# Kernel optimization log

Measured on AMD Instinct MI355X. Metric: run time of the kernel, lower is better.

The kernel has to match this reference:

```python
import jax, jax.numpy as jnp
import numpy as np

B, T, H, TYPE = 32, 512, 1024, 32


def setup_inputs() -> dict:
    key = jax.random.key(0)
    ks = jax.random.split(key, 8)
    s = 0.02
    return {
        "event_seqs": jax.random.randint(ks[0], (B, T), 0, TYPE + 1),
        "time_seqs": jax.random.uniform(ks[1], (B, T), jnp.float32),
        "rec_W": jax.random.normal(ks[2], (2 * H, 7 * H), jnp.float32) * s,
        "rec_b": jnp.zeros((7 * H,), jnp.float32),
        "emb": jax.random.normal(ks[3], (TYPE + 1, H), jnp.float32) * s,
        "w1_W": jax.random.normal(ks[4], (H, H), jnp.float32) * s,
        "w1_b": jnp.zeros((H,), jnp.float32),
        "w2_W": jax.random.normal(ks[5], (H, H), jnp.float32) * s,
        "w2_b": jnp.zeros((H,), jnp.float32),
    }


def reference(event_seqs, time_seqs, rec_W, rec_b, emb, w1_W, w1_b, w2_W, w2_b):
    b, t = event_seqs.shape
    h = emb.shape[1]

    def recurrence(feed_emb, h_d, c_tm1, c_bar_tm1):
        # Linear(2H -> 7H) then gate nonlinearities
        g = jnp.concatenate([feed_emb, h_d], axis=1) @ rec_W + rec_b
        gi, gf, gz, go, gib, gfb, gd = jnp.split(g, 7, axis=-1)
        gz = jnp.tanh(gz)
        c_t = jax.nn.sigmoid(gf) * c_tm1 + jax.nn.sigmoid(gi) * gz
        c_bar_t = jax.nn.sigmoid(gfb) * c_bar_tm1 + jax.nn.sigmoid(gib) * gz
        return c_t, c_bar_t, jax.nn.sigmoid(go), jax.nn.softplus(gd)

    zeros = jnp.zeros((b, h), rec_W.dtype)
    emb0 = jnp.broadcast_to(emb[0], (b, h))  # event_embeddings(zeros)
    carry0 = recurrence(emb0, zeros, zeros, zeros)  # (c, c_bar, o, delta)

    emb_seq = emb[event_seqs].swapaxes(0, 1)  # [T, B, H]
    dur_seq = time_seqs.T                      # [T, B]

    def step(carry, xs):
        c, c_bar, o, delta = carry
        e_t, dur_t = xs
        # exponential decay toward c_bar over the elapsed duration
        c_d = c_bar + (c - c_bar) * jnp.exp(-delta * dur_t[:, None])
        h_d = o * jnp.tanh(c_d)
        return recurrence(e_t, h_d, c_d, c_bar), h_d

    _, h_seq = jax.lax.scan(step, carry0, (emb_seq, dur_seq))  # h_seq: [T, B, H]

    h_last = h_seq[-1]  # last timestep hidden (h.transpose(0,1)[:, -1, :])
    hid = jax.nn.relu(h_last @ w1_W + w1_b)  # dropout = identity (eval)
    return hid @ w2_W + w2_b
```

## Files before the change

### kernel.cpp

```cpp
#include <hip/hip_runtime.h>


#define H   1024
#define B   32
#define T   512
#define NG  7
#define C7  7168
#define K2  2048
#define NWG 256

typedef __attribute__((ext_vector_type(4))) float f32x4;

__device__ __attribute__((aligned(16))) float g_Wt[(size_t)C7 * K2];
__device__ __attribute__((aligned(16))) float g_w1t[(size_t)H * H];
__device__ __attribute__((aligned(16))) float g_w2t[(size_t)H * H];
__device__ __attribute__((aligned(16))) float g_embp[(size_t)33 * C7];
__device__ __attribute__((aligned(16))) float g_hbuf[2][B * H];
__device__ __attribute__((aligned(16))) float g_cd[B * H];
__device__ __attribute__((aligned(16))) float g_cb[B * H];

__device__ __forceinline__ float sig_f(float x){
  return __builtin_amdgcn_rcpf(1.f + __builtin_amdgcn_exp2f(-1.44269504089f * x));
}
__device__ __forceinline__ float tanh_f(float x){
  float t = __builtin_amdgcn_exp2f(2.88539008178f * x);
  return 1.f - 2.f * __builtin_amdgcn_rcpf(t + 1.f);
}
__device__ __forceinline__ float softplus_f(float x){
  float p = __builtin_amdgcn_exp2f(-1.44269504089f * fabsf(x));
  return fmaxf(x, 0.f) + 0.69314718056f * __builtin_amdgcn_logf(1.f + p);
}

template<int C>
__device__ __forceinline__ float dppadd(float a){
  int t = __builtin_amdgcn_mov_dpp(__float_as_int(a), C, 0xF, 0xF, true);
  return a + __int_as_float(t);
}
__device__ __forceinline__ float row16_sum(float a){
  a = dppadd<0xB1>(a);
  a = dppadd<0x4E>(a);
  a = dppadd<0x141>(a);
  a = dppadd<0x140>(a);
  return a;
}

__device__ __forceinline__ float d4(f32x4 a, f32x4 b, float s){
  s = __builtin_fmaf(a.x, b.x, s); s = __builtin_fmaf(a.y, b.y, s);
  s = __builtin_fmaf(a.z, b.z, s); s = __builtin_fmaf(a.w, b.w, s);
  return s;
}

__device__ __forceinline__ void loadrow(const float* src, int ln, f32x4 hv[4]){
  const f32x4* p = (const f32x4*)src;
  #pragma unroll
  for (int i = 0; i < 4; ++i) hv[i] = p[i * 64 + ln];
}

__device__ __forceinline__ void load_wslice(const float* Wbase, int colb, int ln,
                                            int kofs, f32x4 w[NG][4]){
  #pragma unroll
  for (int g = 0; g < NG; ++g){
    const float* cp = Wbase + (size_t)(g * H + colb) * K2 + kofs;
    #pragma unroll
    for (int i = 0; i < 4; ++i) w[g][i] = *(const f32x4*)(cp + (i * 64 + ln) * 4);
  }
}

__device__ __forceinline__ void row_partial(const f32x4 hv[4], const f32x4 w[NG][4],
                                            float* gp, int bi, int wv, int ln){
  float a[NG];
  #pragma unroll
  for (int g = 0; g < NG; ++g){
    float s = 0.f;
    #pragma unroll
    for (int i = 0; i < 4; ++i) s = d4(hv[i], w[g][i], s);
    a[g] = row16_sum(s);
  }
  int m = ln & 15;
  float v = a[0];
  v = (m==1)?a[1]:v; v = (m==2)?a[2]:v; v = (m==3)?a[3]:v;
  v = (m==4)?a[4]:v; v = (m==5)?a[5]:v; v = (m==6)?a[6]:v;
  if (m < NG) gp[bi * 112 + wv * 28 + m * 4 + (ln >> 4)] = v;
}

template<int NR>
__device__ __forceinline__ void mm_block(const float* src, const f32x4 w[NG][4],
                                         float* gp, int wv, int ln){
  f32x4 ha[4], hb[4];
  loadrow(src, ln, ha);
  #pragma unroll
  for (int b = 0; b < NR; b += 2){
    if (b + 1 < NR) loadrow(src + (b + 1) * H, ln, hb);
    row_partial(ha, w, gp, b, wv, ln);
    if (b + 2 < NR) loadrow(src + (b + 2) * H, ln, ha);
    if (b + 1 < NR) row_partial(hb, w, gp, b + 1, wv, ln);
  }
}


extern "C" __global__ void __launch_bounds__(256)
transpose_k(const float* __restrict__ in, int which, int R, int C){
  __shared__ float tls[64 * 65];
  float* out = (which == 0) ? g_Wt : (which == 1 ? g_w1t : g_w2t);
  int tx = threadIdx.x & 63, ty = threadIdx.x >> 6;
  size_t c0 = (size_t)blockIdx.x * 64, r0 = (size_t)blockIdx.y * 64;
  #pragma unroll
  for (int i = 0; i < 16; ++i){
    int r = i * 4 + ty;
    tls[r * 65 + tx] = in[(r0 + r) * (size_t)C + c0 + tx];
  }
  __syncthreads();
  #pragma unroll
  for (int i = 0; i < 16; ++i){
    int c = i * 4 + ty;
    out[(c0 + c) * (size_t)R + r0 + tx] = tls[tx * 65 + c];
  }
}

extern "C" __global__ void __launch_bounds__(256, 1)
embproj_k(const float* __restrict__ emb, const float* __restrict__ recb){
  __shared__ float gp[33 * 112];
  int tid = threadIdx.x, wg = blockIdx.x, wv = tid >> 6, ln = tid & 63;
  int colb = wg * 4 + wv;
  f32x4 w[NG][4];
  load_wslice(g_Wt, colb, ln, 0, w);
  mm_block<33>(emb, w, gp, wv, ln);
  __syncthreads();
  for (int idx = tid; idx < 33 * 4; idx += 256){
    int e = idx >> 2, hl = idx & 3, col = wg * 4 + hl;
    #pragma unroll
    for (int g = 0; g < NG; ++g){
      const float* pp = gp + e * 112 + hl * 28 + g * 4;
      g_embp[(size_t)e * C7 + g * H + col] =
          recb[g * H + col] + ((pp[0] + pp[1]) + (pp[2] + pp[3]));
    }
  }
}

extern "C" __global__ void __launch_bounds__(256)
init_k(const float* __restrict__ tm){
  int tid = threadIdx.x, wg = blockIdx.x;
  if (tid < 128){
    int b = tid >> 2, hl = tid & 3, col = wg * 4 + hl, si = b * H + col;
    float G[NG];
    #pragma unroll
    for (int g = 0; g < NG; ++g) G[g] = g_embp[(size_t)g * H + col];
    float gz = tanh_f(G[2]);
    float c  = sig_f(G[0]) * gz;
    float cb = sig_f(G[4]) * gz;
    float dd = softplus_f(G[6]);
    float dur = tm[b * T];
    float cd = cb + (c - cb) * __builtin_amdgcn_exp2f(-1.44269504089f * dd * dur);
    g_cd[si] = cd; g_cb[si] = cb;
    g_hbuf[0][si] = sig_f(G[3]) * tanh_f(cd);
  }
}

extern "C" __global__ void __launch_bounds__(256, 1)
step_k(int t, const int* __restrict__ ev, const float* __restrict__ tm){
  __shared__ float gp[B * 112];
  int tid = threadIdx.x, wg = blockIdx.x, wv = tid >> 6, ln = tid & 63;
  int colb = wg * 4 + wv;
  f32x4 w[NG][4];
  load_wslice(g_Wt, colb, ln, H, w);
  const float* hprev = g_hbuf[(t - 1) & 1];
  mm_block<B>(hprev, w, gp, wv, ln);
  __syncthreads();
  if (tid < 128){
    int b = tid >> 2, hl = tid & 3, col = wg * 4 + hl, si = b * H + col;
    int e = ev[b * T + t - 1];
    const float* ep = g_embp + (size_t)e * C7 + col;
    float G[NG];
    #pragma unroll
    for (int g = 0; g < NG; ++g){
      const float* pp = gp + b * 112 + hl * 28 + g * 4;
      G[g] = ep[(size_t)g * H] + ((pp[0] + pp[1]) + (pp[2] + pp[3]));
    }
    float gz  = tanh_f(G[2]);
    float cdp = g_cd[si], cbp = g_cb[si];
    float c   = sig_f(G[1]) * cdp + sig_f(G[0]) * gz;
    float cb  = sig_f(G[5]) * cbp + sig_f(G[4]) * gz;
    float dd  = softplus_f(G[6]);
    float dur = tm[b * T + t];
    float cd  = cb + (c - cb) * __builtin_amdgcn_exp2f(-1.44269504089f * dd * dur);
    g_cd[si] = cd; g_cb[si] = cb;
    g_hbuf[t & 1][si] = sig_f(G[3]) * tanh_f(cd);
  }
}

extern "C" __global__ void __launch_bounds__(256, 1)
mlp_k(int phase, const float* __restrict__ bias, float* __restrict__ outp){
  __shared__ float gp[B * 16];
  int tid = threadIdx.x, wg = blockIdx.x, wv = tid >> 6, ln = tid & 63;
  int colb = wg * 4 + wv;
  const float* Wt   = phase ? g_w2t : g_w1t;
  const float* hsrc = phase ? g_hbuf[0] : g_hbuf[1];
  f32x4 w[4];
  #pragma unroll
  for (int i = 0; i < 4; ++i)
    w[i] = *(const f32x4*)(Wt + (size_t)colb * H + (i * 64 + ln) * 4);
  #pragma unroll 2
  for (int b = 0; b < B; ++b){
    f32x4 hv[4]; loadrow(hsrc + b * H, ln, hv);
    float s = 0.f;
    #pragma unroll
    for (int i = 0; i < 4; ++i) s = d4(hv[i], w[i], s);
    s = row16_sum(s);
    if ((ln & 15) == 0) gp[b * 16 + wv * 4 + (ln >> 4)] = s;
  }
  __syncthreads();
  if (tid < 128){
    int b = tid >> 2, hl = tid & 3, col = wg * 4 + hl;
    const float* pp = gp + b * 16 + hl * 4;
    float s = ((pp[0] + pp[1]) + (pp[2] + pp[3])) + bias[col];
    if (!phase) g_hbuf[0][b * H + col] = fmaxf(s, 0.f);
    else        outp[b * H + col] = s;
  }
}

extern "C" void kernel_launch(void* const* d_in, const int* in_sizes, int n_in,
                              void* d_out, int out_size, void* d_ws, size_t ws_size,
                              hipStream_t stream)
{
  const int*   ev = (const int*)  d_in[0];
  const float* tm = (const float*)d_in[1];
  const float* rW = (const float*)d_in[2];
  const float* rb = (const float*)d_in[3];
  const float* em = (const float*)d_in[4];
  const float* w1 = (const float*)d_in[5];
  const float* b1 = (const float*)d_in[6];
  const float* w2 = (const float*)d_in[7];
  const float* b2 = (const float*)d_in[8];
  float* outp = (float*)d_out;
  (void)d_ws; (void)ws_size; (void)in_sizes; (void)n_in; (void)out_size;

  dim3 blk(256);
  hipLaunchKernelGGL(transpose_k, dim3(C7 / 64, K2 / 64), blk, 0, stream, rW, 0, K2, C7);
  hipLaunchKernelGGL(transpose_k, dim3(H / 64, H / 64),  blk, 0, stream, w1, 1, H, H);
  hipLaunchKernelGGL(transpose_k, dim3(H / 64, H / 64),  blk, 0, stream, w2, 2, H, H);
  hipLaunchKernelGGL(embproj_k, dim3(NWG), blk, 0, stream, em, rb);
  hipLaunchKernelGGL(init_k,    dim3(NWG), blk, 0, stream, tm);
  for (int t = 1; t < T; ++t)
    hipLaunchKernelGGL(step_k, dim3(NWG), blk, 0, stream, t, ev, tm);
  hipLaunchKernelGGL(mlp_k, dim3(NWG), blk, 0, stream, 0, b1, outp);
  hipLaunchKernelGGL(mlp_k, dim3(NWG), blk, 0, stream, 1, b2, outp);
}
```

Before: 8.040 ms.

## Replace per-timestep launches with a persistent kernel using flag-based grid barriers

Adds a single persistent kernel that runs all timesteps plus the final MLP. Recurrent weights stay in registers and state stays in LDS across steps, with a spin-flag barrier between workgroups in place of 511 separate kernel launches. It reads weights straight from the untransposed inputs with strided loads, which drops the transpose passes. The spin barrier assumes all 256 workgroups are co-resident, and it has a bounded spin count that could silently break correctness if they are not. The old multi-kernel path remains only as a fallback when the launch fails.

```diff
diff --git a/kernel.cpp b/kernel.cpp
--- a/kernel.cpp
+++ b/kernel.cpp
@@ -18,6 +18,7 @@
 __device__ __attribute__((aligned(16))) float g_hbuf[2][B * H];
 __device__ __attribute__((aligned(16))) float g_cd[B * H];
 __device__ __attribute__((aligned(16))) float g_cb[B * H];
+__device__ unsigned g_flags[NWG];
 
 __device__ __forceinline__ float sig_f(float x){
   return __builtin_amdgcn_rcpf(1.f + __builtin_amdgcn_exp2f(-1.44269504089f * x));
@@ -66,6 +67,20 @@
   }
 }
 
+__device__ __forceinline__ void load_w_direct(const float* recW, int colb, int ln,
+                                              int kofs, f32x4 w[NG][4]){
+  #pragma unroll
+  for (int g = 0; g < NG; ++g)
+    #pragma unroll
+    for (int i = 0; i < 4; ++i){
+      const float* base = recW + (size_t)(kofs + i * 256 + ln * 4) * C7 + g * H + colb;
+      w[g][i].x = base[0];
+      w[g][i].y = base[C7];
+      w[g][i].z = base[2 * C7];
+      w[g][i].w = base[3 * C7];
+    }
+}
+
 __device__ __forceinline__ void row_partial(const f32x4 hv[4], const f32x4 w[NG][4],
                                             float* gp, int bi, int wv, int ln){
   float a[NG];
@@ -97,11 +112,180 @@
   }
 }
 
+__device__ __forceinline__ void flag_barrier(unsigned target, int tid, int bid){
+  __syncthreads();
+  if (tid == 0){
+    __threadfence();
+    __hip_atomic_store(&g_flags[bid], target, __ATOMIC_RELAXED,
+                       __HIP_MEMORY_SCOPE_AGENT);
+  }
+  for (int spin = 0; spin < 32768; ++spin){
+    unsigned v = __hip_atomic_load(&g_flags[tid], __ATOMIC_RELAXED,
+                                   __HIP_MEMORY_SCOPE_AGENT);
+    if ((int)(v - target) >= 0) break;
+    __builtin_amdgcn_s_sleep(1);
+  }
+  __threadfence();
+  __syncthreads();
+}
+
+#define P_TM   0
+#define TMS    520
+#define P_EMBP (32*TMS)
+#define P_GP   (P_EMBP + 33*28)
+#define P_CC   (P_GP + 33*112)
+#define P_CB   (P_CC + 128)
+#define P_OO   (P_CB + 128)
+#define P_DD   (P_OO + 128)
+#define P_CDL  (P_DD + 128)
+#define DYN_LDS_BYTES (21904 * 4)
+
+extern "C" __global__ void __launch_bounds__(256, 1)
+ctlstm_persist(const int* __restrict__ ev, const float* __restrict__ tm,
+               const float* __restrict__ recW, const float* __restrict__ recb,
+               const float* __restrict__ emb,  const float* __restrict__ w1W,
+               const float* __restrict__ w1b,  const float* __restrict__ w2W,
+               const float* __restrict__ w2b,  float* __restrict__ out)
+{
+  extern __shared__ float lds[];
+  const int tid = threadIdx.x, wg = blockIdx.x;
+  const int wv = tid >> 6, ln = tid & 63;
+  const int colb = wg * 4 + wv;
+
+  const unsigned base = __hip_atomic_load(&g_flags[tid], __ATOMIC_RELAXED,
+                                          __HIP_MEMORY_SCOPE_AGENT);
+  unsigned bk = 0;
+
+  for (int i = tid; i < B * T; i += 256){
+    int b = i >> 9, t = i & 511;
+    lds[P_TM + b * TMS + t] = tm[i];
+  }
+
+  f32x4 w[NG][4];
+
+  load_w_direct(recW, colb, ln, 0, w);
+  __syncthreads();
+  mm_block<33>(emb, w, lds + P_GP, wv, ln);
+  __syncthreads();
+  for (int idx = tid; idx < 33 * 4; idx += 256){
+    int e = idx >> 2, hl = idx & 3, col = wg * 4 + hl;
+    #pragma unroll
+    for (int g = 0; g < NG; ++g){
+      const float* pp = lds + P_GP + e * 112 + hl * 28 + g * 4;
+      lds[P_EMBP + e * 28 + g * 4 + hl] =
+          recb[g * H + col] + ((pp[0] + pp[1]) + (pp[2] + pp[3]));
+    }
+  }
+  load_w_direct(recW, colb, ln, H, w);
+  __syncthreads();
+
+  if (tid < 128){
+    int hl = tid & 3, si = tid;
+    float G0 = lds[P_EMBP + 0 * 4 + hl];
+    float G2 = lds[P_EMBP + 2 * 4 + hl];
+    float G3 = lds[P_EMBP + 3 * 4 + hl];
+    float G4 = lds[P_EMBP + 4 * 4 + hl];
+    float G6 = lds[P_EMBP + 6 * 4 + hl];
+    float gz = tanh_f(G2);
+    lds[P_CC + si] = sig_f(G0) * gz;
+    lds[P_OO + si] = sig_f(G3);
+    lds[P_CB + si] = sig_f(G4) * gz;
+    lds[P_DD + si] = softplus_f(G6);
+  }
+  __syncthreads();
+
+  for (int t = 0; t < T; ++t){
+    if (tid < 128){
+      int b = tid >> 2, hl = tid & 3, si = tid;
+      float dur = lds[P_TM + b * TMS + t];
+      float c  = lds[P_CC + si], cb = lds[P_CB + si];
+      float oo = lds[P_OO + si], dd = lds[P_DD + si];
+      float cd = cb + (c - cb) * __builtin_amdgcn_exp2f(-1.44269504089f * dd * dur);
+      lds[P_CDL + si] = cd;
+      g_hbuf[t & 1][b * H + wg * 4 + hl] = oo * tanh_f(cd);
+    }
+    flag_barrier(base + (++bk), tid, wg);
+    if (t == T - 1) break;
+
+    mm_block<B>(g_hbuf[t & 1], w, lds + P_GP, wv, ln);
+    __syncthreads();
+
+    if (tid < 128){
+      int b = tid >> 2, hl = tid & 3, si = tid;
+      int e = ev[b * T + t];
+      const int eb = P_EMBP + e * 28;
+      const int pb = P_GP + b * 112 + hl * 28;
+      float G[NG];
+      #pragma unroll
+      for (int g = 0; g < NG; ++g)
+        G[g] = lds[eb + g * 4 + hl]
+             + ((lds[pb + g * 4 + 0] + lds[pb + g * 4 + 1])
+              + (lds[pb + g * 4 + 2] + lds[pb + g * 4 + 3]));
+      float gz  = tanh_f(G[2]);
+      float cd  = lds[P_CDL + si];
+      float cbo = lds[P_CB + si];
+      lds[P_CC + si] = sig_f(G[1]) * cd  + sig_f(G[0]) * gz;
+      lds[P_CB + si] = sig_f(G[5]) * cbo + sig_f(G[4]) * gz;
+      lds[P_OO + si] = sig_f(G[3]);
+      lds[P_DD + si] = softplus_f(G[6]);
+    }
+  }
+
+  {
+    f32x4 wc[4];
+    #pragma unroll
+    for (int i = 0; i < 4; ++i){
+      const float* bp = w1W + (size_t)(i * 256 + ln * 4) * H + colb;
+      wc[i].x = bp[0]; wc[i].y = bp[H]; wc[i].z = bp[2*H]; wc[i].w = bp[3*H];
+    }
+    #pragma unroll 2
+    for (int b = 0; b < B; ++b){
+      f32x4 hv[4]; loadrow(g_hbuf[1] + b * H, ln, hv);
+      float s = 0.f;
+      #pragma unroll
+      for (int i = 0; i < 4; ++i) s = d4(hv[i], wc[i], s);
+      s = row16_sum(s);
+      if ((ln & 15) == 0) lds[P_GP + b * 16 + wv * 4 + (ln >> 4)] = s;
+    }
+    __syncthreads();
+    if (tid < 128){
+      int b = tid >> 2, hl = tid & 3, col = wg * 4 + hl;
+      const float* pp = lds + P_GP + b * 16 + hl * 4;
+      float s = ((pp[0] + pp[1]) + (pp[2] + pp[3])) + w1b[col];
+      g_hbuf[0][b * H + col] = fmaxf(s, 0.f);
+    }
+  }
+  flag_barrier(base + (++bk), tid, wg);
+  {
+    f32x4 wc[4];
+    #pragma unroll
+    for (int i = 0; i < 4; ++i){
+      const float* bp = w2W + (size_t)(i * 256 + ln * 4) * H + colb;
+      wc[i].x = bp[0]; wc[i].y = bp[H]; wc[i].z = bp[2*H]; wc[i].w = bp[3*H];
+    }
+    #pragma unroll 2
+    for (int b = 0; b < B; ++b){
+      f32x4 hv[4]; loadrow(g_hbuf[0] + b * H, ln, hv);
+      float s = 0.f;
+      #pragma unroll
+      for (int i = 0; i < 4; ++i) s = d4(hv[i], wc[i], s);
+      s = row16_sum(s);
+      if ((ln & 15) == 0) lds[P_GP + b * 16 + wv * 4 + (ln >> 4)] = s;
+    }
+    __syncthreads();
+    if (tid < 128){
+      int b = tid >> 2, hl = tid & 3, col = wg * 4 + hl;
+      const float* pp = lds + P_GP + b * 16 + hl * 4;
+      out[b * H + col] = ((pp[0] + pp[1]) + (pp[2] + pp[3])) + w2b[col];
+    }
+  }
+}
+
 
 extern "C" __global__ void __launch_bounds__(256)
 transpose_k(const float* __restrict__ in, int which, int R, int C){
   __shared__ float tls[64 * 65];
-  float* out = (which == 0) ? g_Wt : (which == 1 ? g_w1t : g_w2t);
+  float* outp = (which == 0) ? g_Wt : (which == 1 ? g_w1t : g_w2t);
   int tx = threadIdx.x & 63, ty = threadIdx.x >> 6;
   size_t c0 = (size_t)blockIdx.x * 64, r0 = (size_t)blockIdx.y * 64;
   #pragma unroll
@@ -113,7 +297,7 @@
   #pragma unroll
   for (int i = 0; i < 16; ++i){
     int c = i * 4 + ty;
-    out[(c0 + c) * (size_t)R + r0 + tx] = tls[tx * 65 + c];
+    outp[(c0 + c) * (size_t)R + r0 + tx] = tls[tx * 65 + c];
   }
 }
 
@@ -234,6 +418,14 @@
   float* outp = (float*)d_out;
   (void)d_ws; (void)ws_size; (void)in_sizes; (void)n_in; (void)out_size;
 
+  hipFuncSetAttribute((const void*)ctlstm_persist,
+                      hipFuncAttributeMaxDynamicSharedMemorySize, DYN_LDS_BYTES);
+
+  (void)hipGetLastError();
+  hipLaunchKernelGGL(ctlstm_persist, dim3(NWG), dim3(256), DYN_LDS_BYTES, stream,
+                     ev, tm, rW, rb, em, w1, b1, w2, b2, outp);
+  if (hipGetLastError() == hipSuccess) return;
+
   dim3 blk(256);
   hipLaunchKernelGGL(transpose_k, dim3(C7 / 64, K2 / 64), blk, 0, stream, rW, 0, K2, C7);
   hipLaunchKernelGGL(transpose_k, dim3(H / 64, H / 64),  blk, 0, stream, w1, 1, H, H);
```

New measurement: 19.09 ms. 2.37x slower.
